# Kernel tuning notes

Measured on AMD Instinct MI355X. Metric: run time of the kernel, lower is better.

## Reference

```python
import jax, jax.numpy as jnp
import numpy as np

IMG = 840.0
MIN_SIZES = [[16.0, 32.0], [64.0, 128.0], [256.0, 512.0]]
STEPS = [8, 16, 32]
THRESH = 0.35      # neg_overlap / matching threshold used by this repo's MultiBoxLoss
NEG_POS = 7
LOC_WEIGHT = 2.0
VAR0, VAR1 = 0.1, 0.2


def _make_priors():
    out = []
    for ms, step in zip(MIN_SIZES, STEPS):
        f = int(np.ceil(IMG / step))
        jj, ii = np.meshgrid(np.arange(f), np.arange(f))  # j: cols (x), i: rows (y)
        cx = (jj + 0.5) * step / IMG
        cy = (ii + 0.5) * step / IMG
        for m in ms:
            s = np.full_like(cx, m / IMG)
            out.append(np.stack([cx, cy, s, s], axis=-1).reshape(-1, 4))
    return np.concatenate(out, axis=0).astype(np.float32)  # [29126, 4] (cx, cy, w, h)


def setup_inputs() -> dict:
    key = jax.random.key(0)
    k1, k2, k3, k4 = jax.random.split(key, 4)
    B, G = 64, 24
    priors = jnp.asarray(_make_priors())            # [P, 4]
    P = priors.shape[0]
    loc_data = 0.1 * jax.random.normal(k1, (B, P, 4), dtype=jnp.float32)
    conf_data = jax.random.normal(k2, (B, P, 2), dtype=jnp.float32)
    cxy = jax.random.uniform(k3, (B, G, 2), minval=0.2, maxval=0.8)
    wh = jax.random.uniform(k4, (B, G, 2), minval=0.05, maxval=0.3)
    gt_boxes = jnp.clip(jnp.concatenate([cxy - wh / 2, cxy + wh / 2], axis=-1), 1e-3, 1.0)
    gt_labels = jnp.ones((B, G), dtype=jnp.int32)   # single foreground class (num_classes=2)
    return {"loc_data": loc_data, "conf_data": conf_data, "gt_boxes": gt_boxes,
            "gt_labels": gt_labels, "priors": priors}


def _multibox_loss(loc_data, conf_data, gt_boxes, gt_labels, priors):
    B, P, _ = loc_data.shape
    G = gt_boxes.shape[1]
    # priors in point form for IoU
    pr_pt = jnp.concatenate([priors[:, :2] - priors[:, 2:] / 2,
                             priors[:, :2] + priors[:, 2:] / 2], axis=1)  # [P,4]
    area_p = (pr_pt[:, 2] - pr_pt[:, 0]) * (pr_pt[:, 3] - pr_pt[:, 1])

    def match_one(truths, labels):
        # IoU [G, P]
        lt = jnp.maximum(truths[:, None, :2], pr_pt[None, :, :2])
        rb = jnp.minimum(truths[:, None, 2:], pr_pt[None, :, 2:])
        wh = jnp.clip(rb - lt, 0.0)
        inter = wh[..., 0] * wh[..., 1]
        area_t = (truths[:, 2] - truths[:, 0]) * (truths[:, 3] - truths[:, 1])
        iou = inter / (area_t[:, None] + area_p[None, :] - inter)
        best_prior_idx = jnp.argmax(iou, axis=1)          # [G]
        bto = jnp.max(iou, axis=0)                        # [P] best truth overlap
        bti = jnp.argmax(iou, axis=0)                     # [P] best truth idx
        bto = bto.at[best_prior_idx].set(2.0)             # ensure each gt keeps its best prior
        bti = bti.at[best_prior_idx].set(jnp.arange(G))
        matched = truths[bti]                             # [P,4]
        conf = jnp.where(bto < THRESH, 0, labels[bti])    # [P]
        # encode (SSD style, variances 0.1/0.2)
        g_cxcy = ((matched[:, :2] + matched[:, 2:]) / 2 - priors[:, :2]) / (VAR0 * priors[:, 2:])
        g_wh = jnp.log((matched[:, 2:] - matched[:, :2]) / priors[:, 2:]) / VAR1
        return jnp.concatenate([g_cxcy, g_wh], axis=1), conf

    loc_t, conf_t = jax.vmap(match_one)(gt_boxes, gt_labels)  # [B,P,4], [B,P]
    pos = conf_t > 0                                          # [B,P]

    # localization: smooth L1 over positives
    diff = jnp.abs(loc_data - loc_t)
    sl1 = jnp.where(diff < 1.0, 0.5 * diff * diff, diff - 0.5)
    loss_l = jnp.sum(sl1 * pos[..., None].astype(loc_data.dtype))

    # per-prior CE = logsumexp - logit[target]
    lse = jax.nn.logsumexp(conf_data, axis=-1)                               # [B,P]
    gold = jnp.take_along_axis(conf_data, conf_t[..., None], axis=-1)[..., 0]
    ce_all = lse - gold                                                      # [B,P]

    # hard negative mining: rank background-class loss of negatives
    mine = jnp.where(pos, 0.0, ce_all)
    rank = jnp.argsort(jnp.argsort(-mine, axis=1), axis=1)
    num_pos = jnp.sum(pos, axis=1, keepdims=True)                            # [B,1]
    num_neg = jnp.minimum(NEG_POS * num_pos, P - 1)
    neg = rank < num_neg

    mask = pos | neg
    loss_c = jnp.sum(jnp.where(mask, ce_all, 0.0))

    N = jnp.maximum(jnp.sum(pos).astype(loc_data.dtype), 1.0)
    return loss_l / N, loss_c / N


def reference(loc_data, conf_data, gt_boxes, gt_labels, priors):
    loss_l, loss_c = _multibox_loss(loc_data, conf_data, gt_boxes, gt_labels, priors)
    return LOC_WEIGHT * loss_l + loss_c
```

## Files before the change

kernel.cpp:

```cpp
#include <hip/hip_runtime.h>

static constexpr int B_ = 64;
static constexpr int P_ = 29126;
static constexpr int G_ = 24;
static constexpr float THRESH_ = 0.35f;
static constexpr int NEGPOS_ = 7;
static constexpr int PBL_ = (P_ + 1023) / 1024;
static constexpr int NBL_ = PBL_ * B_;
static constexpr int CCSTRIDE_ = 32;

__device__ const float LAD_[16] = {
    0.5f,    0.5901f, 0.6964f, 0.8220f, 0.9701f, 1.1450f, 1.3514f, 1.5950f,
    1.8825f, 2.2218f, 2.6223f, 3.0950f, 3.6529f, 4.3113f, 5.0885f, 6.0057f };

static constexpr size_t ZBYTES_ =
    (size_t)B_*P_ + (size_t)B_*CCSTRIDE_*4 + 16;
static constexpr int ZVEC_ = (int)((ZBYTES_ + 15) / 16);

__global__ __launch_bounds__(256) void k_zero(ulonglong2* __restrict__ dst)
{
    const int i = blockIdx.x*256 + threadIdx.x;
    if (i < ZVEC_) dst[i] = make_ulonglong2(0ull, 0ull);
}

__global__ __launch_bounds__(256) void k_sparse(
    const float4* __restrict__ gt4,
    const float4* __restrict__ priors4,
    unsigned char* __restrict__ match,
    unsigned long long* __restrict__ bp_pack)
{
    const int g = blockIdx.x;
    const int b = blockIdx.y;
    const int bg = b*G_ + g;
    const int tid = threadIdx.x;

    const float4 t = gt4[bg];
    const float area_t = (t.z - t.x) * (t.w - t.y);

    float bv = -1.0f; int bq = 0;

#pragma unroll
    for (int r = 0; r < 6; ++r) {
        const int   f    = (r < 2) ? 105 : (r < 4) ? 53 : 27;
        const float sc   = (r < 2) ? 105.0f : (r < 4) ? 52.5f : 26.25f;
        const int   base = (r == 0) ? 0 : (r == 1) ? 11025 : (r == 2) ? 22050
                         : (r == 3) ? 24859 : (r == 4) ? 27668 : 28397;
        const float hw   = ((r == 0) ? 16.0f : (r == 1) ? 32.0f : (r == 2) ? 64.0f
                         : (r == 3) ? 128.0f : (r == 4) ? 256.0f : 512.0f)
                           * (0.5f / 840.0f);

        const int j0 = max(0,     (int)floorf((t.x - hw)*sc - 0.5f) - 1);
        const int j1 = min(f - 1, (int)ceilf ((t.z + hw)*sc - 0.5f) + 1);
        const int i0 = max(0,     (int)floorf((t.y - hw)*sc - 0.5f) - 1);
        const int i1 = min(f - 1, (int)ceilf ((t.w + hw)*sc - 0.5f) + 1);
        const int W = j1 - j0 + 1;
        const int n = W * (i1 - i0 + 1);

        for (int c = tid; c < n; c += 256) {
            const int ii = c / W;
            const int jj = c - ii*W;
            const int p = base + (i0 + ii)*f + (j0 + jj);
            const float4 pr = priors4[p];
            const float hx = pr.z * 0.5f, hy = pr.w * 0.5f;
            const float px0 = pr.x - hx, py0 = pr.y - hy;
            const float px1 = pr.x + hx, py1 = pr.y + hy;
            const float area_p = (px1 - px0) * (py1 - py0);
            const float lx = fmaxf(t.x, px0), ly = fmaxf(t.y, py0);
            const float rx = fminf(t.z, px1), ry = fminf(t.w, py1);
            const float iw = fmaxf(rx - lx, 0.0f), ih = fmaxf(ry - ly, 0.0f);
            const float inter = iw * ih;
            const float iou = __fdividef(inter, (area_t + area_p) - inter);

            if (iou >= THRESH_) match[(size_t)b*P_ + p] = 1;
            if (iou > bv) { bv = iou; bq = p; }
        }
    }

    const int lane = tid & 63, wave = tid >> 6;
    for (int m = 32; m; m >>= 1) {
        const float ov = __shfl_xor(bv, m, 64);
        const int   oq = __shfl_xor(bq, m, 64);
        if (ov > bv || (ov == bv && oq < bq)) { bv = ov; bq = oq; }
    }
    __shared__ float swv[4];
    __shared__ int   swq[4];
    if (lane == 0) { swv[wave] = bv; swq[wave] = bq; }
    __syncthreads();
    if (tid == 0) {
        float v = swv[0]; int q = swq[0];
#pragma unroll
        for (int w = 1; w < 4; ++w)
            if (swv[w] > v || (swv[w] == v && swq[w] < q)) { v = swv[w]; q = swq[w]; }
        bp_pack[bg] = (v >= 0.0f)
            ? (((unsigned long long)__float_as_uint(v) << 32)
               | (unsigned long long)(~(unsigned int)q))
            : 0ull;
    }
}

__global__ __launch_bounds__(256) void k_loss(
    const float4* __restrict__ loc4,
    const float2* __restrict__ conf2,
    const float4* __restrict__ gt4,
    const int* __restrict__ labels,
    const float4* __restrict__ priors4,
    const unsigned char* __restrict__ match,
    const unsigned long long* __restrict__ bp_pack,
    float* __restrict__ mine,
    float* __restrict__ pl, float* __restrict__ pc, int* __restrict__ pp,
    unsigned int* __restrict__ pcnt)
{
    const int b = blockIdx.y;
    const int tid = threadIdx.x;
    const int pbase = blockIdx.x*1024;

    __shared__ float4 sgt[G_];
    __shared__ float  sarea[G_];
    __shared__ int    slab[G_];
    __shared__ signed char sovr[1024];
    if (tid < G_) {
        const float4 t = gt4[b*G_ + tid];
        sgt[tid] = t;
        sarea[tid] = (t.z - t.x) * (t.w - t.y);
        slab[tid] = labels[b*G_ + tid];
    }
    for (int i = tid; i < 1024; i += 256) sovr[i] = -1;
    __syncthreads();
    if (tid == 0) {
        for (int g = 0; g < G_; ++g) {
            const int q = (int)(~(unsigned int)(bp_pack[b*G_ + g] & 0xFFFFFFFFull))
                        - pbase;
            if (q >= 0 && q < 1024) sovr[q] = (signed char)g;
        }
    }
    __syncthreads();

    float lL = 0.0f, pce = 0.0f; int np = 0;
    unsigned q0 = 0, q1 = 0, q2 = 0, q3 = 0, q4 = 0, q5 = 0, q6 = 0, q7 = 0;

#pragma unroll
    for (int c = 0; c < 4; ++c) {
        const int p = pbase + c*256 + tid;
        if (p < P_) {
            const int idx = b*P_ + p;
            const int og = (int)sovr[c*256 + tid];

            int cc = 0, g = 0;
            if (og >= 0) { g = og; cc = slab[g]; }
            else if (match[idx]) {
                const float4 pr = priors4[p];
                const float hx = pr.z * 0.5f, hy = pr.w * 0.5f;
                const float px0 = pr.x - hx, py0 = pr.y - hy;
                const float px1 = pr.x + hx, py1 = pr.y + hy;
                const float area_p = (px1 - px0) * (py1 - py0);
                float best = -1.0f;
#pragma unroll
                for (int gg = 0; gg < G_; ++gg) {
                    const float4 t = sgt[gg];
                    const float lx = fmaxf(t.x, px0), ly = fmaxf(t.y, py0);
                    const float rx = fminf(t.z, px1), ry = fminf(t.w, py1);
                    const float iw = fmaxf(rx - lx, 0.0f), ih = fmaxf(ry - ly, 0.0f);
                    const float inter = iw * ih;
                    const float iou = __fdividef(inter, (sarea[gg] + area_p) - inter);
                    if (iou > best) { best = iou; g = gg; }
                }
                cc = slab[g];
            }

            const float2 x = conf2[idx];
            const float z = (cc == 0) ? (x.y - x.x) : (x.x - x.y);
            const float ce = __logf(1.0f + __expf(z));

            float mv = ce;
            if (cc > 0) {
                np += 1; pce += ce; mv = 0.0f;
                const float4 t  = sgt[g];
                const float4 pr = priors4[p];
                const float gcx = __fdividef((t.x + t.z)*0.5f - pr.x, 0.1f*pr.z);
                const float gcy = __fdividef((t.y + t.w)*0.5f - pr.y, 0.1f*pr.w);
                const float gw  = __logf(__fdividef(t.z - t.x, pr.z)) * 5.0f;
                const float gh  = __logf(__fdividef(t.w - t.y, pr.w)) * 5.0f;
                const float4 l = loc4[idx];
                const float d0 = fabsf(l.x - gcx);
                const float d1 = fabsf(l.y - gcy);
                const float d2 = fabsf(l.z - gw);
                const float d3 = fabsf(l.w - gh);
                lL += (d0 < 1.0f) ? 0.5f*d0*d0 : d0 - 0.5f;
                lL += (d1 < 1.0f) ? 0.5f*d1*d1 : d1 - 0.5f;
                lL += (d2 < 1.0f) ? 0.5f*d2*d2 : d2 - 0.5f;
                lL += (d3 < 1.0f) ? 0.5f*d3*d3 : d3 - 0.5f;
            }
            mine[idx] = mv;

            q0 += (unsigned)(mv > 0.5f)    + ((unsigned)(mv > 0.5901f) << 16);
            q1 += (unsigned)(mv > 0.6964f) + ((unsigned)(mv > 0.8220f) << 16);
            q2 += (unsigned)(mv > 0.9701f) + ((unsigned)(mv > 1.1450f) << 16);
            q3 += (unsigned)(mv > 1.3514f) + ((unsigned)(mv > 1.5950f) << 16);
            q4 += (unsigned)(mv > 1.8825f) + ((unsigned)(mv > 2.2218f) << 16);
            q5 += (unsigned)(mv > 2.6223f) + ((unsigned)(mv > 3.0950f) << 16);
            q6 += (unsigned)(mv > 3.6529f) + ((unsigned)(mv > 4.3113f) << 16);
            q7 += (unsigned)(mv > 5.0885f) + ((unsigned)(mv > 6.0057f) << 16);
        }
    }

    __shared__ float sL[256], sC[256];
    __shared__ int   sP[256];
    __shared__ unsigned su[8][256];
    sL[tid] = lL; sC[tid] = pce; sP[tid] = np;
    su[0][tid] = q0; su[1][tid] = q1; su[2][tid] = q2; su[3][tid] = q3;
    su[4][tid] = q4; su[5][tid] = q5; su[6][tid] = q6; su[7][tid] = q7;
    __syncthreads();
    for (int off = 128; off > 0; off >>= 1) {
        if (tid < off) {
            sL[tid] += sL[tid+off];
            sC[tid] += sC[tid+off];
            sP[tid] += sP[tid+off];
#pragma unroll
            for (int j = 0; j < 8; ++j) su[j][tid] += su[j][tid+off];
        }
        __syncthreads();
    }
    const int o = b*PBL_ + blockIdx.x;
    if (tid == 0) { pl[o] = sL[0]; pc[o] = sC[0]; pp[o] = sP[0]; }
    if (tid < 8) pcnt[o*8 + tid] = su[tid][0];
}

__device__ inline void bracket_block(
    const unsigned int* __restrict__ pcnt, const int* __restrict__ pp,
    int b, int tid, int4* out, int* np_out)
{
    __shared__ int sred[256];
    sred[tid] = (tid < PBL_) ? pp[b*PBL_ + tid] : 0;
    __syncthreads();
    for (int off = 128; off > 0; off >>= 1) {
        if (tid < off) sred[tid] += sred[tid+off];
        __syncthreads();
    }
    const int np = sred[0];
    int k = NEGPOS_ * np; if (k > P_-1) k = P_-1;

    __shared__ unsigned red[32][8];
    {
        const int i = tid >> 3, j = tid & 7;
        red[i][j] = (i < PBL_) ? pcnt[(b*PBL_ + i)*8 + j] : 0u;
    }
    __syncthreads();
    for (int off = 16; off > 0; off >>= 1) {
        const int i = tid >> 3, j = tid & 7;
        if (i < off) red[i][j] += red[i+off][j];
        __syncthreads();
    }
    __shared__ int C[16];
    if (tid < 8) {
        C[2*tid]   = (int)(red[0][tid] & 0xFFFFu);
        C[2*tid+1] = (int)(red[0][tid] >> 16);
    }
    __shared__ int4 sbr;
    __syncthreads();
    if (tid == 0) {
        int4 s; s.w = 0;
        if (k <= 0) {
            s.x = 0x7F800000; s.y = 0x7F800000; s.z = 0;
        } else {
            int js = -1;
            for (int j = 0; j < 16; ++j) if (C[j] >= k) js = j;
            if (js < 0) {
                s.x = __float_as_int(LAD_[0]);
                s.y = __float_as_int(-1.0f);
                s.z = k - C[0];
            } else if (js == 15) {
                s.x = 0x7F800000;
                s.y = __float_as_int(LAD_[15]);
                s.z = k;
            } else {
                s.x = __float_as_int(LAD_[js+1]);
                s.y = __float_as_int(LAD_[js]);
                s.z = k - C[js+1];
            }
        }
        sbr = s;
    }
    __syncthreads();
    *out = sbr;
    *np_out = np;
}

__global__ __launch_bounds__(256) void k_collect(
    const float* __restrict__ mine,
    const unsigned int* __restrict__ pcnt, const int* __restrict__ pp,
    unsigned int* __restrict__ cand, int* __restrict__ candCount,
    float* __restrict__ pcol)
{
    const int b = blockIdx.y;
    const int tid = threadIdx.x;
    const int lane = tid & 63;

    int4 se; int np_dummy;
    bracket_block(pcnt, pp, b, tid, &se, &np_dummy);
    const float hi = __int_as_float(se.x);
    const float lo = __int_as_float(se.y);

    __shared__ unsigned int sbuf[1024];
    __shared__ int scnt;
    __shared__ int gbase;
    if (tid == 0) scnt = 0;
    __syncthreads();

    float sum = 0.0f;
#pragma unroll
    for (int c = 0; c < 4; ++c) {
        const int p = blockIdx.x*1024 + c*256 + tid;
        bool isCand = false;
        unsigned int u = 0;
        if (p < P_) {
            const float v = mine[(size_t)b*P_ + p];
            u = __float_as_uint(v);
            if (v > hi) sum += v;
            else isCand = (v > lo);
        }
        const unsigned long long mask = __ballot(isCand);
        const int wcnt = __popcll(mask);
        int wbase = 0;
        if (lane == 0 && wcnt) wbase = atomicAdd(&scnt, wcnt);
        wbase = __shfl(wbase, 0, 64);
        if (isCand) {
            const int before = __popcll(mask & ((1ull << lane) - 1ull));
            sbuf[wbase + before] = u;
        }
    }
    __syncthreads();
    const int tot = scnt;
    if (tid == 0) gbase = tot ? atomicAdd(&candCount[b*CCSTRIDE_], tot) : 0;
    __syncthreads();
    for (int i = tid; i < tot; i += 256)
        cand[(size_t)b*P_ + gbase + i] = sbuf[i];

    __shared__ float sf2[256];
    sf2[tid] = sum;
    __syncthreads();
    for (int off = 128; off > 0; off >>= 1) {
        if (tid < off) sf2[tid] += sf2[tid+off];
        __syncthreads();
    }
    if (tid == 0) pcol[b*PBL_ + blockIdx.x] = sf2[0];
}

__global__ __launch_bounds__(256) void k_sel2fin(
    const unsigned int* __restrict__ cand, const int* __restrict__ candCount,
    const unsigned int* __restrict__ pcnt, const int* __restrict__ pp,
    const float* __restrict__ pl, const float* __restrict__ pc,
    const float* __restrict__ pcol,
    float4* __restrict__ outb, unsigned int* __restrict__ ticket,
    float* __restrict__ out)
{
    const int b = blockIdx.x;
    const int tid = threadIdx.x;

    int4 se; int np;
    bracket_block(pcnt, pp, b, tid, &se, &np);
    const int kk = se.z;

    __shared__ float rA[256], rB[256], rC2[256];
    rA[tid]  = (tid < PBL_) ? pl[b*PBL_ + tid] : 0.0f;
    rB[tid]  = (tid < PBL_) ? pc[b*PBL_ + tid] : 0.0f;
    rC2[tid] = (tid < PBL_) ? pcol[b*PBL_ + tid] : 0.0f;
    __syncthreads();
    for (int off = 128; off > 0; off >>= 1) {
        if (tid < off) {
            rA[tid] += rA[tid+off];
            rB[tid] += rB[tid+off];
            rC2[tid] += rC2[tid+off];
        }
        __syncthreads();
    }
    const float sumL = rA[0], sumC = rB[0], sumhi = rC2[0];
    __syncthreads();

    float ctopv = sumhi;
    const int nc = candCount[b*CCSTRIDE_];
    if (kk > 0 && nc > 0) {
        const unsigned int* row = cand + (size_t)b * P_;
        __shared__ unsigned int hist[256];
        __shared__ unsigned int sc0[256], sc1[256];
        __shared__ unsigned int sh_prefix;
        __shared__ int sh_kk;

        unsigned int prefix = 0; int kk2 = kk;
        for (int pass = 3; pass >= 0; --pass) {
            hist[tid] = 0;
            __syncthreads();
            const unsigned int highmask =
                (pass == 3) ? 0u : (0xFFFFFFFFu << ((pass+1)*8));
            for (int i = tid; i < nc; i += 256) {
                const unsigned int u = row[i];
                if ((u & highmask) == (prefix & highmask))
                    atomicAdd(&hist[(u >> (pass*8)) & 255u], 1u);
            }
            __syncthreads();
            sc0[tid] = hist[255 - tid];
            __syncthreads();
            unsigned int* src = sc0; unsigned int* dst = sc1;
            for (int off = 1; off < 256; off <<= 1) {
                unsigned int v = src[tid];
                if (tid >= off) v += src[tid - off];
                dst[tid] = v;
                __syncthreads();
                unsigned int* t2 = src; src = dst; dst = t2;
            }
            {
                const int bin = 255 - tid;
                const int cum = (int)src[tid];
                const int cumPrev = (tid == 0) ? 0 : (int)src[tid-1];
                if (cum >= kk2 && cumPrev < kk2) {
                    sh_prefix = prefix | ((unsigned int)bin << (pass*8));
                    sh_kk = kk2 - cumPrev;
                }
            }
            __syncthreads();
            prefix = sh_prefix; kk2 = sh_kk;
            __syncthreads();
        }

        const float T = __uint_as_float(prefix);
        float sum = 0.0f; int cnt = 0;
        for (int i = tid; i < nc; i += 256) {
            const unsigned int u = row[i];
            if (u > prefix) { sum += __uint_as_float(u); ++cnt; }
        }
        __shared__ float sf[256];
        __shared__ int   sci[256];
        sf[tid] = sum; sci[tid] = cnt;
        __syncthreads();
        for (int off = 128; off > 0; off >>= 1) {
            if (tid < off) { sf[tid] += sf[tid+off]; sci[tid] += sci[tid+off]; }
            __syncthreads();
        }
        ctopv = sumhi + sf[0] + (float)(kk - sci[0]) * T;
    }

    __shared__ int sdone;
    if (tid == 0) {
        outb[b] = make_float4(sumL, sumC, (float)np, ctopv);
        __threadfence();
        sdone = (int)atomicAdd(ticket, 1u);
    }
    __syncthreads();
    if (sdone == B_ - 1) {
        __threadfence();
        float L = 0.0f, C = 0.0f, Pn = 0.0f, T = 0.0f;
        if (tid < B_) {
            const float4 v = outb[tid];
            L = v.x; C = v.y; Pn = v.z; T = v.w;
        }
        for (int m = 32; m; m >>= 1) {
            L += __shfl_xor(L, m, 64);
            C += __shfl_xor(C, m, 64);
            Pn += __shfl_xor(Pn, m, 64);
            T += __shfl_xor(T, m, 64);
        }
        if (tid == 0)
            out[0] = (2.0f*L + C + T) / fmaxf(Pn, 1.0f);
    }
}

extern "C" void kernel_launch(void* const* d_in, const int* in_sizes, int n_in,
                              void* d_out, int out_size, void* d_ws, size_t ws_size,
                              hipStream_t stream)
{
    const float* loc    = (const float*)d_in[0];
    const float* conf   = (const float*)d_in[1];
    const float* gt     = (const float*)d_in[2];
    const int*   labels = (const int*)d_in[3];
    const float* priors = (const float*)d_in[4];
    float* out = (float*)d_out;

    char* ws = (char*)d_ws;
    size_t off = 0;
    unsigned char* match = (unsigned char*)(ws + off); off += (size_t)B_*P_;
    int* candCount = (int*)(ws + off);                 off += (size_t)B_*CCSTRIDE_*4;
    unsigned int* ticket = (unsigned int*)(ws + off);  off += 16;
    off = (off + 255) & ~255ull;
    unsigned long long* bp_pack =
        (unsigned long long*)(ws + off);             off += (size_t)B_*G_*8;
    float* mine = (float*)(ws + off);                off += (size_t)B_*P_*4;
    float* pl   = (float*)(ws + off);                off += (size_t)NBL_*4;
    float* pc   = (float*)(ws + off);                off += (size_t)NBL_*4;
    int*   pp   = (int*)(ws + off);                  off += (size_t)NBL_*4;
    float* pcol = (float*)(ws + off);                off += (size_t)NBL_*4;
    unsigned int* pcnt = (unsigned int*)(ws + off);  off += (size_t)NBL_*8*4;
    unsigned int* cand = (unsigned int*)(ws + off);  off += (size_t)B_*P_*4;
    float4* outb = (float4*)(ws + off);              off += (size_t)B_*16;

    k_zero<<<dim3((ZVEC_ + 255)/256), dim3(256), 0, stream>>>((ulonglong2*)ws);
    k_sparse<<<dim3(G_, B_), dim3(256), 0, stream>>>(
        (const float4*)gt, (const float4*)priors, match, bp_pack);
    k_loss<<<dim3(PBL_, B_), dim3(256), 0, stream>>>(
        (const float4*)loc, (const float2*)conf, (const float4*)gt, labels,
        (const float4*)priors, match, bp_pack, mine, pl, pc, pp, pcnt);
    k_collect<<<dim3(PBL_, B_), dim3(256), 0, stream>>>(
        mine, pcnt, pp, cand, candCount, pcol);
    k_sel2fin<<<dim3(B_), dim3(256), 0, stream>>>(
        cand, candCount, pcnt, pp, pl, pc, pcol, outb, ticket, out);
}
```

Measured before the change: 76.34 us.

## Pack match flags into bitmask and vectorize per-thread 4-prior processing

Replaces the per-prior byte match array with a bitmask set via atomicOr, which shrinks the buffer k_zero must clear from about 1.9MB to about 230KB. k_loss now has each thread handle four contiguous priors, using float4 loads of conf and float4 stores into a padded mine buffer, and k_collect reads mine with float4 loads. The override map is built in parallel with atomicMax instead of by a single thread. The risks are atomic contention on the bitmask words and a changed tie-break: the highest g now wins where the old serial loop let the last write win. The per-thread branchy IoU fallback may also diverge more.

Result: slower. 79.61 us (+4.3%).

```diff
diff --git a/kernel.cpp b/kernel.cpp
--- a/kernel.cpp
+++ b/kernel.cpp
@@ -6,15 +6,17 @@
 static constexpr float THRESH_ = 0.35f;
 static constexpr int NEGPOS_ = 7;
 static constexpr int PBL_ = (P_ + 1023) / 1024;
+static constexpr int PPAD_ = PBL_ * 1024;
 static constexpr int NBL_ = PBL_ * B_;
-static constexpr int CCSTRIDE_ = 32;
+static constexpr int WPB_ = 912;
+static constexpr int CCS_ = 32;
 
 __device__ const float LAD_[16] = {
     0.5f,    0.5901f, 0.6964f, 0.8220f, 0.9701f, 1.1450f, 1.3514f, 1.5950f,
     1.8825f, 2.2218f, 2.6223f, 3.0950f, 3.6529f, 4.3113f, 5.0885f, 6.0057f };
 
 static constexpr size_t ZBYTES_ =
-    (size_t)B_*P_ + (size_t)B_*CCSTRIDE_*4 + 16;
+    (size_t)B_*WPB_*4 + (size_t)B_*CCS_*4 + 16;
 static constexpr int ZVEC_ = (int)((ZBYTES_ + 15) / 16);
 
 __global__ __launch_bounds__(256) void k_zero(ulonglong2* __restrict__ dst)
@@ -26,7 +28,7 @@
 __global__ __launch_bounds__(256) void k_sparse(
     const float4* __restrict__ gt4,
     const float4* __restrict__ priors4,
-    unsigned char* __restrict__ match,
+    unsigned* __restrict__ matchw,
     unsigned long long* __restrict__ bp_pack)
 {
     const int g = blockIdx.x;
@@ -71,7 +73,8 @@
             const float inter = iw * ih;
             const float iou = __fdividef(inter, (area_t + area_p) - inter);
 
-            if (iou >= THRESH_) match[(size_t)b*P_ + p] = 1;
+            if (iou >= THRESH_)
+                atomicOr(&matchw[b*WPB_ + (p >> 5)], 1u << (p & 31));
             if (iou > bv) { bv = iou; bq = p; }
         }
     }
@@ -104,7 +107,7 @@
     const float4* __restrict__ gt4,
     const int* __restrict__ labels,
     const float4* __restrict__ priors4,
-    const unsigned char* __restrict__ match,
+    const unsigned* __restrict__ matchw,
     const unsigned long long* __restrict__ bp_pack,
     float* __restrict__ mine,
     float* __restrict__ pl, float* __restrict__ pc, int* __restrict__ pp,
@@ -117,7 +120,7 @@
     __shared__ float4 sgt[G_];
     __shared__ float  sarea[G_];
     __shared__ int    slab[G_];
-    __shared__ signed char sovr[1024];
+    __shared__ int    sovr[1024];
     if (tid < G_) {
         const float4 t = gt4[b*G_ + tid];
         sgt[tid] = t;
@@ -126,80 +129,107 @@
     }
     for (int i = tid; i < 1024; i += 256) sovr[i] = -1;
     __syncthreads();
-    if (tid == 0) {
-        for (int g = 0; g < G_; ++g) {
-            const int q = (int)(~(unsigned int)(bp_pack[b*G_ + g] & 0xFFFFFFFFull))
-                        - pbase;
-            if (q >= 0 && q < 1024) sovr[q] = (signed char)g;
-        }
-    }
-    __syncthreads();
-
+    if (tid < G_) {
+        const unsigned long long pk = bp_pack[b*G_ + tid];
+        const int q = (int)(~(unsigned int)(pk & 0xFFFFFFFFull)) - pbase;
+        if (q >= 0 && q < 1024) atomicMax(&sovr[q], tid);
+    }
+    __syncthreads();
+
+    const int p0 = pbase + tid*4;
     float lL = 0.0f, pce = 0.0f; int np = 0;
     unsigned q0 = 0, q1 = 0, q2 = 0, q3 = 0, q4 = 0, q5 = 0, q6 = 0, q7 = 0;
+    float m4[4] = {0.0f, 0.0f, 0.0f, 0.0f};
+
+    if (p0 < P_) {
+        const unsigned mw = matchw[b*WPB_ + (p0 >> 5)] >> (p0 & 31);
+        const bool full = (p0 + 3 < P_);
+
+        float cf[8];
+        if (full) {
+            const float4* c4 = (const float4*)conf2;
+            const size_t base2 = ((size_t)b*P_ + p0) >> 1;
+            const float4 ca = c4[base2];
+            const float4 cb = c4[base2 + 1];
+            cf[0]=ca.x; cf[1]=ca.y; cf[2]=ca.z; cf[3]=ca.w;
+            cf[4]=cb.x; cf[5]=cb.y; cf[6]=cb.z; cf[7]=cb.w;
+        } else {
+            for (int c = 0; c < 4; ++c) {
+                if (p0 + c < P_) {
+                    const float2 x = conf2[(size_t)b*P_ + p0 + c];
+                    cf[2*c] = x.x; cf[2*c+1] = x.y;
+                } else { cf[2*c] = 0.0f; cf[2*c+1] = 0.0f; }
+            }
+        }
 
 #pragma unroll
-    for (int c = 0; c < 4; ++c) {
-        const int p = pbase + c*256 + tid;
-        if (p < P_) {
-            const int idx = b*P_ + p;
-            const int og = (int)sovr[c*256 + tid];
-
-            int cc = 0, g = 0;
-            if (og >= 0) { g = og; cc = slab[g]; }
-            else if (match[idx]) {
-                const float4 pr = priors4[p];
-                const float hx = pr.z * 0.5f, hy = pr.w * 0.5f;
-                const float px0 = pr.x - hx, py0 = pr.y - hy;
-                const float px1 = pr.x + hx, py1 = pr.y + hy;
-                const float area_p = (px1 - px0) * (py1 - py0);
-                float best = -1.0f;
+        for (int c = 0; c < 4; ++c) {
+            const int p = p0 + c;
+            if (p < P_) {
+                const int og = sovr[tid*4 + c];
+                int cc = 0, g = 0;
+                if (og >= 0) { g = og; cc = slab[g]; }
+                else if ((mw >> c) & 1u) {
+                    const float4 pr = priors4[p];
+                    const float hx = pr.z * 0.5f, hy = pr.w * 0.5f;
+                    const float px0 = pr.x - hx, py0 = pr.y - hy;
+                    const float px1 = pr.x + hx, py1 = pr.y + hy;
+                    const float area_p = (px1 - px0) * (py1 - py0);
+                    float best = -1.0f;
 #pragma unroll
-                for (int gg = 0; gg < G_; ++gg) {
-                    const float4 t = sgt[gg];
-                    const float lx = fmaxf(t.x, px0), ly = fmaxf(t.y, py0);
-                    const float rx = fminf(t.z, px1), ry = fminf(t.w, py1);
-                    const float iw = fmaxf(rx - lx, 0.0f), ih = fmaxf(ry - ly, 0.0f);
-                    const float inter = iw * ih;
-                    const float iou = __fdividef(inter, (sarea[gg] + area_p) - inter);
-                    if (iou > best) { best = iou; g = gg; }
+                    for (int gg = 0; gg < G_; ++gg) {
+                        const float4 t = sgt[gg];
+                        const float lx = fmaxf(t.x, px0), ly = fmaxf(t.y, py0);
+                        const float rx = fminf(t.z, px1), ry = fminf(t.w, py1);
+                        const float iw = fmaxf(rx - lx, 0.0f), ih = fmaxf(ry - ly, 0.0f);
+                        const float inter = iw * ih;
+                        const float iou = __fdividef(inter, (sarea[gg] + area_p) - inter);
+                        if (iou > best) { best = iou; g = gg; }
+                    }
+                    cc = slab[g];
                 }
-                cc = slab[g];
+
+                const float z = (cc == 0) ? (cf[2*c+1] - cf[2*c])
+                                          : (cf[2*c] - cf[2*c+1]);
+                const float ce = __logf(1.0f + __expf(z));
+
+                float m = ce;
+                if (cc > 0) {
+                    np += 1; pce += ce; m = 0.0f;
+                    const float4 t  = sgt[g];
+                    const float4 pr = priors4[p];
+                    const float gcx = __fdividef((t.x + t.z)*0.5f - pr.x, 0.1f*pr.z);
+                    const float gcy = __fdividef((t.y + t.w)*0.5f - pr.y, 0.1f*pr.w);
+                    const float gw  = __logf(__fdividef(t.z - t.x, pr.z)) * 5.0f;
+                    const float gh  = __logf(__fdividef(t.w - t.y, pr.w)) * 5.0f;
+                    const float4 l = loc4[(size_t)b*P_ + p];
+                    const float d0 = fabsf(l.x - gcx);
+                    const float d1 = fabsf(l.y - gcy);
+                    const float d2 = fabsf(l.z - gw);
+                    const float d3 = fabsf(l.w - gh);
+                    lL += (d0 < 1.0f) ? 0.5f*d0*d0 : d0 - 0.5f;
+                    lL += (d1 < 1.0f) ? 0.5f*d1*d1 : d1 - 0.5f;
+                    lL += (d2 < 1.0f) ? 0.5f*d2*d2 : d2 - 0.5f;
+                    lL += (d3 < 1.0f) ? 0.5f*d3*d3 : d3 - 0.5f;
+                }
+                m4[c] = m;
+                q0 += (unsigned)(m > 0.5f)    + ((unsigned)(m > 0.5901f) << 16);
+                q1 += (unsigned)(m > 0.6964f) + ((unsigned)(m > 0.8220f) << 16);
+                q2 += (unsigned)(m > 0.9701f) + ((unsigned)(m > 1.1450f) << 16);
+                q3 += (unsigned)(m > 1.3514f) + ((unsigned)(m > 1.5950f) << 16);
+                q4 += (unsigned)(m > 1.8825f) + ((unsigned)(m > 2.2218f) << 16);
+                q5 += (unsigned)(m > 2.6223f) + ((unsigned)(m > 3.0950f) << 16);
+                q6 += (unsigned)(m > 3.6529f) + ((unsigned)(m > 4.3113f) << 16);
+                q7 += (unsigned)(m > 5.0885f) + ((unsigned)(m > 6.0057f) << 16);
             }
-
-            const float2 x = conf2[idx];
-            const float z = (cc == 0) ? (x.y - x.x) : (x.x - x.y);
-            const float ce = __logf(1.0f + __expf(z));
-
-            float mv = ce;
-            if (cc > 0) {
-                np += 1; pce += ce; mv = 0.0f;
-                const float4 t  = sgt[g];
-                const float4 pr = priors4[p];
-                const float gcx = __fdividef((t.x + t.z)*0.5f - pr.x, 0.1f*pr.z);
-                const float gcy = __fdividef((t.y + t.w)*0.5f - pr.y, 0.1f*pr.w);
-                const float gw  = __logf(__fdividef(t.z - t.x, pr.z)) * 5.0f;
-                const float gh  = __logf(__fdividef(t.w - t.y, pr.w)) * 5.0f;
-                const float4 l = loc4[idx];
-                const float d0 = fabsf(l.x - gcx);
-                const float d1 = fabsf(l.y - gcy);
-                const float d2 = fabsf(l.z - gw);
-                const float d3 = fabsf(l.w - gh);
-                lL += (d0 < 1.0f) ? 0.5f*d0*d0 : d0 - 0.5f;
-                lL += (d1 < 1.0f) ? 0.5f*d1*d1 : d1 - 0.5f;
-                lL += (d2 < 1.0f) ? 0.5f*d2*d2 : d2 - 0.5f;
-                lL += (d3 < 1.0f) ? 0.5f*d3*d3 : d3 - 0.5f;
-            }
-            mine[idx] = mv;
-
-            q0 += (unsigned)(mv > 0.5f)    + ((unsigned)(mv > 0.5901f) << 16);
-            q1 += (unsigned)(mv > 0.6964f) + ((unsigned)(mv > 0.8220f) << 16);
-            q2 += (unsigned)(mv > 0.9701f) + ((unsigned)(mv > 1.1450f) << 16);
-            q3 += (unsigned)(mv > 1.3514f) + ((unsigned)(mv > 1.5950f) << 16);
-            q4 += (unsigned)(mv > 1.8825f) + ((unsigned)(mv > 2.2218f) << 16);
-            q5 += (unsigned)(mv > 2.6223f) + ((unsigned)(mv > 3.0950f) << 16);
-            q6 += (unsigned)(mv > 3.6529f) + ((unsigned)(mv > 4.3113f) << 16);
-            q7 += (unsigned)(mv > 5.0885f) + ((unsigned)(mv > 6.0057f) << 16);
+        }
+
+        float* mrow = mine + (size_t)b*PPAD_ + p0;
+        if (full) {
+            *(float4*)mrow = make_float4(m4[0], m4[1], m4[2], m4[3]);
+        } else {
+            for (int c = 0; c < 4; ++c)
+                if (p0 + c < P_) mrow[c] = m4[c];
         }
     }
 
@@ -306,18 +336,23 @@
     if (tid == 0) scnt = 0;
     __syncthreads();
 
+    const int p0 = blockIdx.x*1024 + tid*4;
+    float v4[4] = {-1.0f, -1.0f, -1.0f, -1.0f};
+    if (p0 + 3 < P_) {
+        const float4 v = *(const float4*)(mine + (size_t)b*PPAD_ + p0);
+        v4[0] = v.x; v4[1] = v.y; v4[2] = v.z; v4[3] = v.w;
+    } else if (p0 < P_) {
+        for (int c = 0; c < 4; ++c)
+            if (p0 + c < P_) v4[c] = mine[(size_t)b*PPAD_ + p0 + c];
+    }
+
     float sum = 0.0f;
 #pragma unroll
     for (int c = 0; c < 4; ++c) {
-        const int p = blockIdx.x*1024 + c*256 + tid;
+        const float v = v4[c];
         bool isCand = false;
-        unsigned int u = 0;
-        if (p < P_) {
-            const float v = mine[(size_t)b*P_ + p];
-            u = __float_as_uint(v);
-            if (v > hi) sum += v;
-            else isCand = (v > lo);
-        }
+        if (v > hi) sum += v;
+        else isCand = (v > lo);
         const unsigned long long mask = __ballot(isCand);
         const int wcnt = __popcll(mask);
         int wbase = 0;
@@ -325,12 +360,12 @@
         wbase = __shfl(wbase, 0, 64);
         if (isCand) {
             const int before = __popcll(mask & ((1ull << lane) - 1ull));
-            sbuf[wbase + before] = u;
+            sbuf[wbase + before] = __float_as_uint(v);
         }
     }
     __syncthreads();
     const int tot = scnt;
-    if (tid == 0) gbase = tot ? atomicAdd(&candCount[b*CCSTRIDE_], tot) : 0;
+    if (tid == 0) gbase = tot ? atomicAdd(&candCount[b*CCS_], tot) : 0;
     __syncthreads();
     for (int i = tid; i < tot; i += 256)
         cand[(size_t)b*P_ + gbase + i] = sbuf[i];
@@ -377,7 +412,7 @@
     __syncthreads();
 
     float ctopv = sumhi;
-    const int nc = candCount[b*CCSTRIDE_];
+    const int nc = candCount[b*CCS_];
     if (kk > 0 && nc > 0) {
         const unsigned int* row = cand + (size_t)b * P_;
         __shared__ unsigned int hist[256];
@@ -476,13 +511,13 @@
 
     char* ws = (char*)d_ws;
     size_t off = 0;
-    unsigned char* match = (unsigned char*)(ws + off); off += (size_t)B_*P_;
-    int* candCount = (int*)(ws + off);                 off += (size_t)B_*CCSTRIDE_*4;
-    unsigned int* ticket = (unsigned int*)(ws + off);  off += 16;
+    unsigned* matchw = (unsigned*)(ws + off);        off += (size_t)B_*WPB_*4;
+    int* candCount = (int*)(ws + off);               off += (size_t)B_*CCS_*4;
+    unsigned int* ticket = (unsigned int*)(ws + off); off += 16;
     off = (off + 255) & ~255ull;
     unsigned long long* bp_pack =
         (unsigned long long*)(ws + off);             off += (size_t)B_*G_*8;
-    float* mine = (float*)(ws + off);                off += (size_t)B_*P_*4;
+    float* mine = (float*)(ws + off);                off += (size_t)B_*PPAD_*4;
     float* pl   = (float*)(ws + off);                off += (size_t)NBL_*4;
     float* pc   = (float*)(ws + off);                off += (size_t)NBL_*4;
     int*   pp   = (int*)(ws + off);                  off += (size_t)NBL_*4;
@@ -493,10 +528,10 @@
 
     k_zero<<<dim3((ZVEC_ + 255)/256), dim3(256), 0, stream>>>((ulonglong2*)ws);
     k_sparse<<<dim3(G_, B_), dim3(256), 0, stream>>>(
-        (const float4*)gt, (const float4*)priors, match, bp_pack);
+        (const float4*)gt, (const float4*)priors, matchw, bp_pack);
     k_loss<<<dim3(PBL_, B_), dim3(256), 0, stream>>>(
         (const float4*)loc, (const float2*)conf, (const float4*)gt, labels,
-        (const float4*)priors, match, bp_pack, mine, pl, pc, pp, pcnt);
+        (const float4*)priors, matchw, bp_pack, mine, pl, pc, pp, pcnt);
     k_collect<<<dim3(PBL_, B_), dim3(256), 0, stream>>>(
         mine, pcnt, pp, cand, candCount, pcol);
     k_sel2fin<<<dim3(B_), dim3(256), 0, stream>>>(
```
